# Kernel tuning notes

Hardware: AMD Instinct MI355X
Metric: run time of the kernel (lower is better)

## Reference

```python
import jax, jax.numpy as jnp
import numpy as np

NP_ = 20000   # paper nodes
NA_ = 20000   # author nodes
E_AP = 400000
E_PP = 400000
D_IN, D_H, HEADS, D_HEAD, D_FF, D_OUT = 128, 256, 8, 32, 2048, 64


def setup_inputs() -> dict:
    key = jax.random.key(0)
    ks = iter(jax.random.split(key, 48))
    def nrm(shape, s=0.1):
        return jax.random.normal(next(ks), shape, jnp.float32) * s
    inp = {
        'feat_paper': nrm((NP_, D_IN), 1.0),
        'feat_author': nrm((NA_, D_IN), 1.0),
        'W_in_p': nrm((D_H, D_IN)), 'b_in_p': nrm((D_H,), 0.05),
        'W_in_a': nrm((D_H, D_IN)), 'b_in_a': nrm((D_H,), 0.05),
        'W_gat_ap': nrm((D_H, D_H)), 'al_ap': nrm((HEADS, D_HEAD)), 'ar_ap': nrm((HEADS, D_HEAD)), 'b_gat_ap': nrm((D_H,), 0.05),
        'W_gat_pp': nrm((D_H, D_H)), 'al_pp': nrm((HEADS, D_HEAD)), 'ar_pp': nrm((HEADS, D_HEAD)), 'b_gat_pp': nrm((D_H,), 0.05),
        'Wqkv_s': nrm((3 * D_H, D_H)), 'bqkv_s': nrm((3 * D_H,), 0.05), 'Wo_s': nrm((D_H, D_H)), 'bo_s': nrm((D_H,), 0.05),
        'Wqkv_c': nrm((3 * D_H, D_H)), 'bqkv_c': nrm((3 * D_H,), 0.05), 'Wo_c': nrm((D_H, D_H)), 'bo_c': nrm((D_H,), 0.05),
        'W_ff1': nrm((D_FF, D_H)), 'b_ff1': nrm((D_FF,), 0.05),
        'W_ff2': nrm((D_H, D_FF)), 'b_ff2': nrm((D_H,), 0.05),
        'ln1_g': jnp.ones((D_H,), jnp.float32), 'ln1_b': jnp.zeros((D_H,), jnp.float32),
        'ln2_g': jnp.ones((D_H,), jnp.float32), 'ln2_b': jnp.zeros((D_H,), jnp.float32),
        'ln3_g': jnp.ones((D_H,), jnp.float32), 'ln3_b': jnp.zeros((D_H,), jnp.float32),
        'W_pred': nrm((D_OUT, 3 * D_H)), 'b_pred': nrm((D_OUT,), 0.05),
        'ap_src': jax.random.randint(next(ks), (E_AP,), 0, NA_),
        'ap_dst': jax.random.randint(next(ks), (E_AP,), 0, NP_),
        'pp_src': jax.random.randint(next(ks), (E_PP,), 0, NP_),
        'pp_dst': jax.random.randint(next(ks), (E_PP,), 0, NP_),
    }
    return inp


def _leaky(x):
    return jnp.where(x > 0, x, 0.2 * x)  # DGL GATConv negative_slope=0.2


def _gat(x, src, dst, W, al, ar, b):
    """DGL GATConv on homogeneous graph with self-loops appended (eval mode)."""
    N = x.shape[0]
    h = (x @ W.T).reshape(N, HEADS, D_HEAD)          # fc has no bias in GATConv
    el = (h * al[None]).sum(-1)                      # (N, H)
    er = (h * ar[None]).sum(-1)                      # (N, H)
    sl = jnp.arange(N, dtype=src.dtype)              # self loops (add_self_loop)
    s = jnp.concatenate([src, sl])
    d = jnp.concatenate([dst, sl])
    e = _leaky(el[s] + er[d])                        # (E+N, H)
    m = jax.ops.segment_max(e, d, num_segments=N)    # edge-softmax per dst
    a = jnp.exp(e - m[d])
    z = jax.ops.segment_sum(a, d, num_segments=N)
    out = jax.ops.segment_sum(a[:, :, None] * h[s], d, num_segments=N)
    out = out / z[:, :, None] + b.reshape(1, HEADS, D_HEAD)
    return out.reshape(N, D_H)                       # flatten(start_dim=1)


def _ln(x, g, b):
    mu = x.mean(-1, keepdims=True)
    v = ((x - mu) ** 2).mean(-1, keepdims=True)
    return (x - mu) / jnp.sqrt(v + 1e-5) * g + b


def _mha(xq, xkv, Wqkv, bqkv, Wo, bo):
    Wq, Wk, Wv = jnp.split(Wqkv, 3, axis=0)
    bq, bk, bv = jnp.split(bqkv, 3)
    B, S, _ = xq.shape
    Sk = xkv.shape[1]
    q = (xq @ Wq.T + bq).reshape(B, S, HEADS, D_HEAD)
    k = (xkv @ Wk.T + bk).reshape(B, Sk, HEADS, D_HEAD)
    v = (xkv @ Wv.T + bv).reshape(B, Sk, HEADS, D_HEAD)
    att = jnp.einsum('bqhd,bkhd->bhqk', q, k) * (D_HEAD ** -0.5)
    a = jax.nn.softmax(att, axis=-1)
    o = jnp.einsum('bhqk,bkhd->bqhd', a, v).reshape(B, S, D_H)
    return o @ Wo.T + bo


def reference(feat_paper, feat_author, W_in_p, b_in_p, W_in_a, b_in_a,
              W_gat_ap, al_ap, ar_ap, b_gat_ap, W_gat_pp, al_pp, ar_pp, b_gat_pp,
              Wqkv_s, bqkv_s, Wo_s, bo_s, Wqkv_c, bqkv_c, Wo_c, bo_c,
              W_ff1, b_ff1, W_ff2, b_ff2, ln1_g, ln1_b, ln2_g, ln2_b, ln3_g, ln3_b,
              W_pred, b_pred, ap_src, ap_dst, pp_src, pp_dst):
    # fc_in per node type
    hp = feat_paper @ W_in_p.T + b_in_p              # (NP, D_H)
    ha = feat_author @ W_in_a.T + b_in_a             # (NA, D_H)
    Na = ha.shape[0]
    # etype 'ap': bipartite author->paper, to_homogeneous orders [author; paper]
    x_ap = jnp.concatenate([ha, hp], axis=0)
    out_ap = _gat(x_ap, ap_src, ap_dst + Na, W_gat_ap, al_ap, ar_ap, b_gat_ap)[Na:]
    # etype 'pp': paper->paper (single node set)
    out_pp = _gat(hp, pp_src, pp_dst, W_gat_pp, al_pp, ar_pp, b_gat_pp)
    # h dict order: 'paper', 'paper-author', 'paper-paper'
    tgt = jnp.stack([hp, out_ap, out_pp], axis=1)    # (NP, 3, D_H)
    # TransformerDecoderLayer (post-norm, relu, eval): memory = tgt
    x = _ln(tgt + _mha(tgt, tgt, Wqkv_s, bqkv_s, Wo_s, bo_s), ln1_g, ln1_b)
    x = _ln(x + _mha(x, tgt, Wqkv_c, bqkv_c, Wo_c, bo_c), ln2_g, ln2_b)
    ff = jax.nn.relu(x @ W_ff1.T + b_ff1) @ W_ff2.T + b_ff2
    z = _ln(x + ff, ln3_g, ln3_b)
    return z.reshape(z.shape[0], -1) @ W_pred.T + b_pred
```

## Files before the change

### kernel.cpp

```cpp
#include <hip/hip_runtime.h>
#include <hip/hip_bf16.h>
#include <cstdint>
#include <cstddef>

#define NP_N 20000
#define NA_N 20000
#define E_AP_N 400000
#define E_PP_N 400000

typedef __attribute__((ext_vector_type(8))) short bf16x8;
typedef __attribute__((ext_vector_type(4))) float f32x4;

__device__ __forceinline__ float b2f(ushort u) { return __uint_as_float(((uint32_t)u) << 16); }
__device__ __forceinline__ ushort f2b(float f) {
    uint32_t x = __float_as_uint(f);
    return (ushort)((x + 0x7fffu + ((x >> 16) & 1u)) >> 16);
}

#define LGKM_BARRIER() do { \
    asm volatile("s_waitcnt lgkmcnt(0)" ::: "memory"); \
    __builtin_amdgcn_s_barrier(); \
    __builtin_amdgcn_sched_barrier(0); \
} while (0)

#define NJOBS 14
struct PackJobs {
    const float* src[NJOBS];
    void* dst[NJOBS];
    int M[NJOBS], K[NJOBS];
    int type[NJOBS];
    int nquad[NJOBS];
    int blk0[NJOBS];
};

__global__ void pack_all_kernel(PackJobs J)
{
    int b = blockIdx.x;
    int j = 0;
    while (j + 1 < NJOBS && b >= J.blk0[j + 1]) ++j;
    int u = (b - J.blk0[j]) * 256 + threadIdx.x;
    if (u >= J.nquad[j]) return;
    int ty = J.type[j];
    const float* src = J.src[j];
    if (ty == 3) {
        float4 v = ((const float4*)src)[u];
        ushort4 o;
        o.x = f2b(v.x); o.y = f2b(v.y); o.z = f2b(v.z); o.w = f2b(v.w);
        ((ushort4*)J.dst[j])[u] = o;
    } else if (ty == 4) {
        int4 z = {0, 0, 0, 0};
        ((int4*)J.dst[j])[u] = z;
    } else if (ty == 0) {
        int M = J.M[j], K = J.K[j];
        int KT = K >> 5;
        int q = u & 1023;
        int jt = u >> 10;
        int t = jt % KT, jj = jt / KT;
        int ks = q >> 8, rem = q & 255;
        int r = rem >> 1;
        int e0 = (rem & 1) * 4;
        int row = jj * 128 + r;
        ushort4 o = {0, 0, 0, 0};
        if (row < M) {
            const float* s = src + (size_t)row * K + t * 32 + ks * 8 + e0;
            o.x = f2b(s[0]); o.y = f2b(s[1]); o.z = f2b(s[2]); o.w = f2b(s[3]);
        }
        ((ushort4*)J.dst[j])[u] = o;
    } else if (ty == 1) {
        int q = u & 2047, chunk = u >> 11;
        int s = q >> 6, rem = q & 63;
        int fl = rem >> 1, e0 = (rem & 1) * 4;
        const float* sp = src + (size_t)(chunk * 32 + fl) * 256 + s * 8 + e0;
        ushort4 o;
        o.x = f2b(sp[0]); o.y = f2b(sp[1]); o.z = f2b(sp[2]); o.w = f2b(sp[3]);
        ((ushort4*)J.dst[j])[u] = o;
    } else {
        int q = u & 2047, chunk = u >> 11;
        int s2 = q >> 9, rem = q & 511;
        int c = rem >> 1, e0 = (rem & 1) * 4;
        const float* sp = src + (size_t)c * 2048 + chunk * 32 + s2 * 8 + e0;
        ushort4 o;
        o.x = f2b(sp[0]); o.y = f2b(sp[1]); o.z = f2b(sp[2]); o.w = f2b(sp[3]);
        ((ushort4*)J.dst[j])[u] = o;
    }
}

__device__ __forceinline__ void gemm_body_bf16(
    ushort* Ab, ushort* Bb,
    const ushort* A, const ushort* Bp, const float* bias, ushort* C,
    int N, int M, int K, int lda, int ldc, int row0, int col0)
{
    const int tid = threadIdx.x;
    const int lane = tid & 63;
    const int w = tid >> 6;
    const int wr = w >> 1, wc = w & 1;
    const int KT = K >> 5;
    const ushort* Bbase = Bp + (size_t)(col0 >> 7) * KT * 4096;
    f32x4 acc[4][4] = {};

    size_t aoff[2];
#pragma unroll
    for (int i = 0; i < 2; ++i) {
        int r = row0 + i * 64 + lane;
        if (r > N - 1) r = N - 1;
        aoff[i] = (size_t)r * lda + w * 8;
    }

    auto stage = [&](int buf, int t) {
        const int k0 = t << 5;
#pragma unroll
        for (int i = 0; i < 2; ++i) {
            __builtin_amdgcn_global_load_lds(
                (const __attribute__((address_space(1))) void*)(A + aoff[i] + k0),
                (__attribute__((address_space(3))) void*)(&Ab[buf * 4096 + (w * 2 + i) * 512]), 16, 0, 0);
        }
#pragma unroll
        for (int i = 0; i < 2; ++i) {
            __builtin_amdgcn_global_load_lds(
                (const __attribute__((address_space(1))) void*)(Bbase + (size_t)t * 4096 + (w * 2 + i) * 512 + lane * 8),
                (__attribute__((address_space(3))) void*)(&Bb[buf * 4096 + (w * 2 + i) * 512]), 16, 0, 0);
        }
    };

    stage(0, 0);
    stage(1, 1);

    int cur = 0;
    for (int t = 0; t < KT; ++t) {
        if (t + 1 < KT) { asm volatile("s_waitcnt vmcnt(4)" ::: "memory"); }
        else            { asm volatile("s_waitcnt vmcnt(0)" ::: "memory"); }
        __builtin_amdgcn_s_barrier();
        __builtin_amdgcn_sched_barrier(0);
        if (t + 2 < KT) {
            int nb = cur - 1; if (nb < 0) nb = 2;
            stage(nb, t + 2);
        }

        bf16x8 af[4], bfr[4];
        const int ks = lane >> 4;
        const int rl = lane & 15;
#pragma unroll
        for (int m = 0; m < 4; ++m)
            af[m] = *(const bf16x8*)&Ab[cur * 4096 + ks * 1024 + (wr * 64 + m * 16 + rl) * 8];
#pragma unroll
        for (int n = 0; n < 4; ++n)
            bfr[n] = *(const bf16x8*)&Bb[cur * 4096 + ks * 1024 + (wc * 64 + n * 16 + rl) * 8];
#pragma unroll
        for (int m = 0; m < 4; ++m)
#pragma unroll
            for (int n = 0; n < 4; ++n)
                acc[m][n] = __builtin_amdgcn_mfma_f32_16x16x32_bf16(af[m], bfr[n], acc[m][n], 0, 0, 0);

        cur = (cur == 2) ? 0 : cur + 1;
    }

#pragma unroll
    for (int m = 0; m < 4; ++m) {
#pragma unroll
        for (int n = 0; n < 4; ++n) {
            int gc = col0 + wc * 64 + n * 16 + (lane & 15);
            if (gc >= M) continue;
            float bv = bias ? bias[gc] : 0.f;
#pragma unroll
            for (int r = 0; r < 4; ++r) {
                int grow = row0 + wr * 64 + m * 16 + (lane >> 4) * 4 + r;
                if (grow >= N) continue;
                C[(size_t)grow * ldc + gc] = f2b(acc[m][n][r] + bv);
            }
        }
    }
}

template <int OUT_MODE>
__global__ __launch_bounds__(256) void gemm_mfma(
    const ushort* __restrict__ A, const ushort* __restrict__ Bp,
    const float* __restrict__ bias, void* __restrict__ Cv,
    int N, int M, int K, int lda, int ldc)
{
    __shared__ __align__(16) ushort Ab[3 * 4096];
    __shared__ __align__(16) ushort Bb[3 * 4096];
    if (OUT_MODE == 0) {
        gemm_body_bf16(Ab, Bb, A, Bp, bias, (ushort*)Cv, N, M, K, lda, ldc,
                       blockIdx.x * 128, blockIdx.y * 128);
        return;
    }
    const int tid = threadIdx.x;
    const int lane = tid & 63;
    const int w = tid >> 6;
    const int wr = w >> 1, wc = w & 1;
    const int row0 = blockIdx.x * 128;
    const int col0 = blockIdx.y * 128;
    const int KT = K >> 5;
    const ushort* Bbase = Bp + (size_t)blockIdx.y * KT * 4096;
    f32x4 acc[4][4] = {};

    size_t aoff[2];
#pragma unroll
    for (int i = 0; i < 2; ++i) {
        int r = row0 + i * 64 + lane;
        if (r > N - 1) r = N - 1;
        aoff[i] = (size_t)r * lda + w * 8;
    }

    auto stage = [&](int buf, int t) {
        const int k0 = t << 5;
#pragma unroll
        for (int i = 0; i < 2; ++i) {
            __builtin_amdgcn_global_load_lds(
                (const __attribute__((address_space(1))) void*)(A + aoff[i] + k0),
                (__attribute__((address_space(3))) void*)(&Ab[buf * 4096 + (w * 2 + i) * 512]), 16, 0, 0);
        }
#pragma unroll
        for (int i = 0; i < 2; ++i) {
            __builtin_amdgcn_global_load_lds(
                (const __attribute__((address_space(1))) void*)(Bbase + (size_t)t * 4096 + (w * 2 + i) * 512 + lane * 8),
                (__attribute__((address_space(3))) void*)(&Bb[buf * 4096 + (w * 2 + i) * 512]), 16, 0, 0);
        }
    };

    stage(0, 0);
    stage(1, 1);

    int cur = 0;
    for (int t = 0; t < KT; ++t) {
        if (t + 1 < KT) { asm volatile("s_waitcnt vmcnt(4)" ::: "memory"); }
        else            { asm volatile("s_waitcnt vmcnt(0)" ::: "memory"); }
        __builtin_amdgcn_s_barrier();
        __builtin_amdgcn_sched_barrier(0);
        if (t + 2 < KT) {
            int nb = cur - 1; if (nb < 0) nb = 2;
            stage(nb, t + 2);
        }

        bf16x8 af[4], bfr[4];
        const int ks = lane >> 4;
        const int rl = lane & 15;
#pragma unroll
        for (int m = 0; m < 4; ++m)
            af[m] = *(const bf16x8*)&Ab[cur * 4096 + ks * 1024 + (wr * 64 + m * 16 + rl) * 8];
#pragma unroll
        for (int n = 0; n < 4; ++n)
            bfr[n] = *(const bf16x8*)&Bb[cur * 4096 + ks * 1024 + (wc * 64 + n * 16 + rl) * 8];
#pragma unroll
        for (int m = 0; m < 4; ++m)
#pragma unroll
            for (int n = 0; n < 4; ++n)
                acc[m][n] = __builtin_amdgcn_mfma_f32_16x16x32_bf16(af[m], bfr[n], acc[m][n], 0, 0, 0);

        cur = (cur == 2) ? 0 : cur + 1;
    }

#pragma unroll
    for (int m = 0; m < 4; ++m) {
#pragma unroll
        for (int n = 0; n < 4; ++n) {
            int gc = col0 + wc * 64 + n * 16 + (lane & 15);
            if (gc >= M) continue;
            float bv = bias ? bias[gc] : 0.f;
#pragma unroll
            for (int r = 0; r < 4; ++r) {
                int grow = row0 + wr * 64 + m * 16 + (lane >> 4) * 4 + r;
                if (grow >= N) continue;
                ((float*)Cv)[(size_t)grow * ldc + gc] = acc[m][n][r] + bv;
            }
        }
    }
}

static inline void gemm_bf(const ushort* A, const ushort* Bp, const float* bias, void* C,
                           int N, int M, int K, int lda, int ldc, int mode, hipStream_t s)
{
    dim3 g((N + 127) / 128, (M + 127) / 128);
    if (mode == 0) gemm_mfma<0><<<g, 256, 0, s>>>(A, Bp, bias, C, N, M, K, lda, ldc);
    else           gemm_mfma<1><<<g, 256, 0, s>>>(A, Bp, bias, C, N, M, K, lda, ldc);
}

#define GNJ 3
struct GemmJobs {
    const ushort* A[GNJ];
    const ushort* Bp[GNJ];
    const float* bias[GNJ];
    ushort* C[GNJ];
    int N[GNJ], M[GNJ], K[GNJ], lda[GNJ], ldc[GNJ];
    int blk0[GNJ], nbx[GNJ];
    int njobs;
};

__global__ __launch_bounds__(256) void gemm_batch_kernel(GemmJobs G)
{
    __shared__ __align__(16) ushort Ab[3 * 4096];
    __shared__ __align__(16) ushort Bb[3 * 4096];
    int b = blockIdx.x;
    int j = 0;
    while (j + 1 < G.njobs && b >= G.blk0[j + 1]) ++j;
    int lb = b - G.blk0[j];
    int bx = lb % G.nbx[j];
    int by = lb / G.nbx[j];
    gemm_body_bf16(Ab, Bb, G.A[j], G.Bp[j], G.bias[j], G.C[j],
                   G.N[j], G.M[j], G.K[j], G.lda[j], G.ldc[j], bx * 128, by * 128);
}

__global__ __launch_bounds__(256, 2) void proj_ln_kernel(
    const ushort* o, int ldo,
    const ushort* __restrict__ Bp, const float* __restrict__ bo,
    const ushort* res, int ldr,
    const float* __restrict__ g, const float* __restrict__ be,
    ushort* X, int N)
{
    __shared__ __align__(16) ushort Wb[8192];
    const int tid = threadIdx.x;
    const int lane = tid & 63;
    const int w = tid >> 6;
    const int wr = w >> 1, wc = w & 1;
    const int row0 = blockIdx.x * 64;
    const int rl = lane & 15;
    const int ks = lane >> 4;

    int arow[2];
#pragma unroll
    for (int m = 0; m < 2; ++m) {
        int r = row0 + wr * 32 + m * 16 + rl;
        arow[m] = (r < N) ? r : (N - 1);
    }

    f32x4 oacc[2][8] = {};

    for (int t = 0; t < 8; ++t) {
#pragma unroll
        for (int i = 0; i < 4; ++i) {
            int ii = w * 4 + i;
            const ushort* src = Bp + ((size_t)(ii >> 3) * 8 + t) * 4096 + (ii & 7) * 512 + lane * 8;
            __builtin_amdgcn_global_load_lds(
                (const __attribute__((address_space(1))) void*)src,
                (__attribute__((address_space(3))) void*)(&Wb[ii * 512]), 16, 0, 0);
        }
        bf16x8 af[2];
#pragma unroll
        for (int m = 0; m < 2; ++m)
            af[m] = *(const bf16x8*)(o + (size_t)arow[m] * ldo + t * 32 + ks * 8);
        __syncthreads();

#pragma unroll
        for (int n = 0; n < 8; ++n) {
            bf16x8 bfr = *(const bf16x8*)&Wb[wc * 4096 + ks * 1024 + (n * 16 + rl) * 8];
#pragma unroll
            for (int m = 0; m < 2; ++m)
                oacc[m][n] = __builtin_amdgcn_mfma_f32_16x16x32_bf16(af[m], bfr, oacc[m][n], 0, 0, 0);
        }
        __syncthreads();
    }

    float2* lnb = (float2*)Wb;
    float psum[2][4] = {}, psq[2][4] = {};
#pragma unroll
    for (int n = 0; n < 8; ++n) {
        int c = wc * 128 + n * 16 + rl;
        float bv = bo[c];
#pragma unroll
        for (int m = 0; m < 2; ++m)
#pragma unroll
            for (int r = 0; r < 4; ++r) {
                int grow = row0 + wr * 32 + m * 16 + ks * 4 + r;
                float v = oacc[m][n][r] + bv + b2f(res[(size_t)grow * ldr + c]);
                oacc[m][n][r] = v;
                psum[m][r] += v;
                psq[m][r] = fmaf(v, v, psq[m][r]);
            }
    }
#pragma unroll
    for (int off = 8; off >= 1; off >>= 1)
#pragma unroll
        for (int m = 0; m < 2; ++m)
#pragma unroll
            for (int r = 0; r < 4; ++r) {
                psum[m][r] += __shfl_xor(psum[m][r], off);
                psq[m][r]  += __shfl_xor(psq[m][r], off);
            }
    if (rl == 0) {
#pragma unroll
        for (int m = 0; m < 2; ++m)
#pragma unroll
            for (int r = 0; r < 4; ++r) {
                int lr = wr * 32 + m * 16 + ks * 4 + r;
                lnb[wc * 64 + lr] = make_float2(psum[m][r], psq[m][r]);
            }
    }
    __syncthreads();
    float mean_[2][4], rstd_[2][4];
#pragma unroll
    for (int m = 0; m < 2; ++m)
#pragma unroll
        for (int r = 0; r < 4; ++r) {
            int lr = wr * 32 + m * 16 + ks * 4 + r;
            float2 a0 = lnb[lr], a1 = lnb[64 + lr];
            float mean = (a0.x + a1.x) * (1.f / 256.f);
            float var = (a0.y + a1.y) * (1.f / 256.f) - mean * mean;
            mean_[m][r] = mean;
            rstd_[m][r] = rsqrtf(var + 1e-5f);
        }
#pragma unroll
    for (int n = 0; n < 8; ++n) {
        int c = wc * 128 + n * 16 + rl;
        float gv = g[c], bev = be[c];
#pragma unroll
        for (int m = 0; m < 2; ++m)
#pragma unroll
            for (int r = 0; r < 4; ++r) {
                int grow = row0 + wr * 32 + m * 16 + ks * 4 + r;
                if (grow < N)
                    X[(size_t)grow * 256 + c] =
                        f2b((oacc[m][n][r] - mean_[m][r]) * rstd_[m][r] * gv + bev);
            }
    }
}

__global__ __launch_bounds__(256, 2) void ff_ln_kernel(
    const ushort* __restrict__ W1p, const ushort* __restrict__ W2p,
    const float* __restrict__ b1, const float* __restrict__ b2,
    const float* __restrict__ g3, const float* __restrict__ be3,
    ushort* X, int N)
{
    __shared__ __align__(16) ushort W1buf[8192];
    __shared__ __align__(16) ushort W2buf[8192];
    __shared__ __align__(16) ushort Sbuf[2048];
    const int tid = threadIdx.x;
    const int lane = tid & 63;
    const int w = tid >> 6;
    const int wr = w >> 1, wc = w & 1;
    const int row0 = blockIdx.x * 64;
    const int rl = lane & 15;
    const int ks = lane >> 4;

    bf16x8 xf[2][8];
#pragma unroll
    for (int m = 0; m < 2; ++m) {
        int gr = row0 + wr * 32 + m * 16 + rl;
        if (gr > N - 1) gr = N - 1;
        const ushort* xrow = X + (size_t)gr * 256 + ks * 8;
#pragma unroll
        for (int kc = 0; kc < 8; ++kc)
            xf[m][kc] = *(const bf16x8*)(xrow + kc * 32);
    }

    f32x4 oacc[2][8] = {};

    for (int fc = 0; fc < 64; ++fc) {
#pragma unroll
        for (int i = 0; i < 8; ++i) {
            int ii = w * 8 + i;
            const ushort* src;
            ushort* dst;
            if (ii < 16) {
                src = W1p + (size_t)fc * 8192 + ii * 512 + lane * 8;
                dst = &W1buf[ii * 512];
            } else {
                src = W2p + (size_t)fc * 8192 + (ii - 16) * 512 + lane * 8;
                dst = &W2buf[(ii - 16) * 512];
            }
            __builtin_amdgcn_global_load_lds(
                (const __attribute__((address_space(1))) void*)src,
                (__attribute__((address_space(3))) void*)dst, 16, 0, 0);
        }
        __syncthreads();

        f32x4 sacc[2] = {};
#pragma unroll
        for (int kc = 0; kc < 8; ++kc) {
            bf16x8 w1f = *(const bf16x8*)&W1buf[(kc * 4 + ks) * 256 + (wc * 16 + rl) * 8];
#pragma unroll
            for (int m = 0; m < 2; ++m)
                sacc[m] = __builtin_amdgcn_mfma_f32_16x16x32_bf16(w1f, xf[m][kc], sacc[m], 0, 0, 0);
        }
        {
            const int f0 = fc * 32;
            const int fb = wc * 16 + ks * 4;
            const int sidx = wc * 2 + (ks >> 1);
            const int e0 = (ks & 1) * 4;
            float4 b1v = *(const float4*)&b1[f0 + fb];
#pragma unroll
            for (int m = 0; m < 2; ++m) {
                ushort4 o;
                o.x = f2b(fmaxf(sacc[m][0] + b1v.x, 0.f));
                o.y = f2b(fmaxf(sacc[m][1] + b1v.y, 0.f));
                o.z = f2b(fmaxf(sacc[m][2] + b1v.z, 0.f));
                o.w = f2b(fmaxf(sacc[m][3] + b1v.w, 0.f));
                *(ushort4*)&Sbuf[(sidx * 64 + wr * 32 + m * 16 + rl) * 8 + e0] = o;
            }
        }
        LGKM_BARRIER();

        {
            bf16x8 sf[2];
#pragma unroll
            for (int m = 0; m < 2; ++m)
                sf[m] = *(const bf16x8*)&Sbuf[ks * 512 + (wr * 32 + m * 16 + rl) * 8];
#pragma unroll
            for (int n = 0; n < 8; ++n) {
                bf16x8 w2f = *(const bf16x8*)&W2buf[ks * 2048 + (wc * 128 + n * 16 + rl) * 8];
#pragma unroll
                for (int m = 0; m < 2; ++m)
                    oacc[m][n] = __builtin_amdgcn_mfma_f32_16x16x32_bf16(sf[m], w2f, oacc[m][n], 0, 0, 0);
            }
        }
        __syncthreads();
    }

    float2* lnb = (float2*)W1buf;
    float psum[2][4] = {}, psq[2][4] = {};
#pragma unroll
    for (int n = 0; n < 8; ++n) {
        int c = wc * 128 + n * 16 + rl;
        float bv = b2[c];
#pragma unroll
        for (int m = 0; m < 2; ++m)
#pragma unroll
            for (int r = 0; r < 4; ++r) {
                int grow = row0 + wr * 32 + m * 16 + ks * 4 + r;
                float v = oacc[m][n][r] + bv + b2f(X[(size_t)grow * 256 + c]);
                oacc[m][n][r] = v;
                psum[m][r] += v;
                psq[m][r] = fmaf(v, v, psq[m][r]);
            }
    }
#pragma unroll
    for (int off = 8; off >= 1; off >>= 1)
#pragma unroll
        for (int m = 0; m < 2; ++m)
#pragma unroll
            for (int r = 0; r < 4; ++r) {
                psum[m][r] += __shfl_xor(psum[m][r], off);
                psq[m][r]  += __shfl_xor(psq[m][r], off);
            }
    if (rl == 0) {
#pragma unroll
        for (int m = 0; m < 2; ++m)
#pragma unroll
            for (int r = 0; r < 4; ++r) {
                int lr = wr * 32 + m * 16 + ks * 4 + r;
                lnb[wc * 64 + lr] = make_float2(psum[m][r], psq[m][r]);
            }
    }
    __syncthreads();
    float mean_[2][4], rstd_[2][4];
#pragma unroll
    for (int m = 0; m < 2; ++m)
#pragma unroll
        for (int r = 0; r < 4; ++r) {
            int lr = wr * 32 + m * 16 + ks * 4 + r;
            float2 a0 = lnb[lr], a1 = lnb[64 + lr];
            float mean = (a0.x + a1.x) * (1.f / 256.f);
            float var = (a0.y + a1.y) * (1.f / 256.f) - mean * mean;
            mean_[m][r] = mean;
            rstd_[m][r] = rsqrtf(var + 1e-5f);
        }
#pragma unroll
    for (int n = 0; n < 8; ++n) {
        int c = wc * 128 + n * 16 + rl;
        float gv = g3[c], bev = be3[c];
#pragma unroll
        for (int m = 0; m < 2; ++m)
#pragma unroll
            for (int r = 0; r < 4; ++r) {
                int grow = row0 + wr * 32 + m * 16 + ks * 4 + r;
                if (grow < N)
                    X[(size_t)grow * 256 + c] =
                        f2b((oacc[m][n][r] - mean_[m][r]) * rstd_[m][r] * gv + bev);
            }
    }
}

__global__ void attn_lr_all_kernel(
    const ushort* __restrict__ h0, const float* __restrict__ al0, const float* __restrict__ ar0,
    float* __restrict__ el0, float* __restrict__ er0,
    const ushort* __restrict__ h1, const float* __restrict__ al1, const float* __restrict__ ar1,
    float* __restrict__ el1, float* __restrict__ er1)
{
    int idx = blockIdx.x * blockDim.x + threadIdx.x;
    if (idx >= 480000) return;
    const ushort* h; const float *a1, *a2; float *el, *er; int i;
    if (idx < 320000) { h = h0; a1 = al0; a2 = ar0; el = el0; er = er0; i = idx; }
    else { h = h1; a1 = al1; a2 = ar1; el = el1; er = er1; i = idx - 320000; }
    int hd = i & 7;
    const ushort* hp = h + (size_t)(i >> 3) * 256 + hd * 32;
    const float* p1 = a1 + hd * 32;
    const float* p2 = a2 + hd * 32;
    float s1 = 0.f, s2 = 0.f;
#pragma unroll
    for (int j = 0; j < 8; ++j) {
        ushort4 t = ((const ushort4*)hp)[j];
        float v0 = b2f(t.x), v1 = b2f(t.y), v2 = b2f(t.z), v3 = b2f(t.w);
        s1 = fmaf(v0, p1[j * 4 + 0], s1); s2 = fmaf(v0, p2[j * 4 + 0], s2);
        s1 = fmaf(v1, p1[j * 4 + 1], s1); s2 = fmaf(v1, p2[j * 4 + 1], s2);
        s1 = fmaf(v2, p1[j * 4 + 2], s1); s2 = fmaf(v2, p2[j * 4 + 2], s2);
        s1 = fmaf(v3, p1[j * 4 + 3], s1); s2 = fmaf(v3, p2[j * 4 + 3], s2);
    }
    el[i] = s1;
    er[i] = s2;
}

__global__ void count2_kernel(const int* __restrict__ d0, int* __restrict__ c0,
                              const int* __restrict__ d1, int* __restrict__ c1, int E)
{
    int e = blockIdx.x * blockDim.x + threadIdx.x;
    if (e < E) atomicAdd(&c0[d0[e]], 1);
    else if (e < 2 * E) atomicAdd(&c1[d1[e - E]], 1);
}

__global__ void scan_chunk_kernel(const int* __restrict__ deg0, int* __restrict__ offs0,
                                  const int* __restrict__ deg1, int* __restrict__ offs1,
                                  int* __restrict__ parts, int N)
{
    int es = blockIdx.x / 20, ch = blockIdx.x % 20;
    const int* deg = es ? deg1 : deg0;
    int* offs = es ? offs1 : offs0;
    __shared__ int sbuf[1024];
    int tid = threadIdx.x;
    int i = ch * 1024 + tid;
    int v = (i < N) ? deg[i] : 0;
    sbuf[tid] = v;
    __syncthreads();
    for (int off = 1; off < 1024; off <<= 1) {
        int t = (tid >= off) ? sbuf[tid - off] : 0;
        __syncthreads();
        sbuf[tid] += t;
        __syncthreads();
    }
    if (i < N) offs[i] = sbuf[tid] - v;
    if (tid == 1023) parts[es * 21 + ch] = sbuf[1023];
}

__global__ void scan_final_kernel(int* __restrict__ deg0, int* __restrict__ offs0,
                                  int* __restrict__ deg1, int* __restrict__ offs1,
                                  const int* __restrict__ parts, int N)
{
    int es = blockIdx.x / 20, ch = blockIdx.x % 20;
    int* deg = es ? deg1 : deg0;
    int* offs = es ? offs1 : offs0;
    __shared__ int base_s, tot_s;
    int tid = threadIdx.x;
    if (tid == 0) {
        const int* p = parts + es * 21;
        int acc = 0, base = 0;
        for (int i = 0; i < 20; ++i) { if (i == ch) base = acc; acc += p[i]; }
        base_s = base;
        tot_s = acc;
    }
    __syncthreads();
    int i = ch * 1024 + tid;
    if (i < N) { offs[i] += base_s; deg[i] = 0; }
    if (ch == 19 && tid == 1023) offs[N] = tot_s;
}

__global__ void scatter2_kernel(const int* __restrict__ s0, const int* __restrict__ d0,
                                const int* __restrict__ o0, int* __restrict__ c0, int* __restrict__ l0,
                                const int* __restrict__ s1, const int* __restrict__ d1,
                                const int* __restrict__ o1, int* __restrict__ c1, int* __restrict__ l1,
                                int E)
{
    int e = blockIdx.x * blockDim.x + threadIdx.x;
    if (e < E) {
        int d = d0[e];
        int pos = atomicAdd(&c0[d], 1);
        l0[o0[d] + pos] = s0[e];
    } else if (e < 2 * E) {
        int e1 = e - E;
        int d = d1[e1];
        int pos = atomicAdd(&c1[d], 1);
        l1[o1[d] + pos] = s1[e1];
    }
}

__global__ __launch_bounds__(64) void gat_agg_all_kernel(
    const ushort* __restrict__ ha, const float* __restrict__ ela, const float* __restrict__ era,
    const int* __restrict__ offsa, const int* __restrict__ lista, const float* __restrict__ biasa,
    const ushort* __restrict__ hp, const float* __restrict__ elp, const float* __restrict__ erp,
    const int* __restrict__ offsp, const int* __restrict__ listp, const float* __restrict__ biasp,
    ushort* __restrict__ out)
{
    int bid = blockIdx.x;
    const ushort* h; const float *el, *er, *bias; const int *offs, *elist;
    int p, dn, coloff;
    if (bid < NP_N) {
        h = ha; el = ela; er = era; offs = offsa; elist = lista; bias = biasa;
        p = bid; dn = NA_N + p; coloff = 256;
    } else {
        h = hp; el = elp; er = erp; offs = offsp; elist = listp; bias = biasp;
        p = bid - NP_N; dn = p; coloff = 512;
    }
    int l = threadIdx.x;
    int head = l >> 3;
    float erv = er[(size_t)dn * 8 + head];
    float acc[4] = {0.f, 0.f, 0.f, 0.f};
    float z = 0.f;
    int beg = offs[p], end = offs[p + 1];
    for (int e = beg - 1; e < end; ++e) {
        int s = (e < beg) ? dn : elist[e];
        float x = el[(size_t)s * 8 + head] + erv;
        x = x > 0.f ? x : 0.2f * x;
        float wgt = expf(x);
        z += wgt;
        ushort4 hv = *(const ushort4*)&h[(size_t)s * 256 + l * 4];
        acc[0] = fmaf(wgt, b2f(hv.x), acc[0]);
        acc[1] = fmaf(wgt, b2f(hv.y), acc[1]);
        acc[2] = fmaf(wgt, b2f(hv.z), acc[2]);
        acc[3] = fmaf(wgt, b2f(hv.w), acc[3]);
    }
    float inv = 1.f / z;
    ushort4 o;
    o.x = f2b(acc[0] * inv + bias[l * 4 + 0]);
    o.y = f2b(acc[1] * inv + bias[l * 4 + 1]);
    o.z = f2b(acc[2] * inv + bias[l * 4 + 2]);
    o.w = f2b(acc[3] * inv + bias[l * 4 + 3]);
    *(ushort4*)&out[(size_t)p * 768 + coloff + l * 4] = o;
}

__global__ void mha3_kernel(const ushort* qb, int ldq, int qoff,
                            const ushort* kvb, int ldkv, int koff, int voff,
                            ushort* ob, int ldo, int NPn)
{
    int idx = blockIdx.x * blockDim.x + threadIdx.x;
    if (idx >= NPn * 24) return;
    int h = idx & 7;
    int i = (idx >> 3) % 3;
    int p = idx / 24;
    float qr[32];
    {
        const ushort* q = qb + (size_t)(p * 3 + i) * ldq + qoff + h * 32;
#pragma unroll
        for (int j = 0; j < 8; ++j) {
            ushort4 t = ((const ushort4*)q)[j];
            qr[j * 4 + 0] = b2f(t.x); qr[j * 4 + 1] = b2f(t.y);
            qr[j * 4 + 2] = b2f(t.z); qr[j * 4 + 3] = b2f(t.w);
        }
    }
    float s[3];
#pragma unroll
    for (int j = 0; j < 3; ++j) {
        const ushort* k = kvb + (size_t)(p * 3 + j) * ldkv + koff + h * 32;
        float a = 0.f;
#pragma unroll
        for (int t4 = 0; t4 < 8; ++t4) {
            ushort4 t = ((const ushort4*)k)[t4];
            a = fmaf(qr[t4 * 4 + 0], b2f(t.x), a);
            a = fmaf(qr[t4 * 4 + 1], b2f(t.y), a);
            a = fmaf(qr[t4 * 4 + 2], b2f(t.z), a);
            a = fmaf(qr[t4 * 4 + 3], b2f(t.w), a);
        }
        s[j] = a * 0.17677669529663687f;
    }
    float m = fmaxf(s[0], fmaxf(s[1], s[2]));
    float e0 = expf(s[0] - m), e1 = expf(s[1] - m), e2 = expf(s[2] - m);
    float inv = 1.f / (e0 + e1 + e2);
    float aw[3] = {e0 * inv, e1 * inv, e2 * inv};
    float o[32] = {};
#pragma unroll
    for (int j = 0; j < 3; ++j) {
        const ushort* v = kvb + (size_t)(p * 3 + j) * ldkv + voff + h * 32;
#pragma unroll
        for (int t4 = 0; t4 < 8; ++t4) {
            ushort4 t = ((const ushort4*)v)[t4];
            o[t4 * 4 + 0] = fmaf(aw[j], b2f(t.x), o[t4 * 4 + 0]);
            o[t4 * 4 + 1] = fmaf(aw[j], b2f(t.y), o[t4 * 4 + 1]);
            o[t4 * 4 + 2] = fmaf(aw[j], b2f(t.z), o[t4 * 4 + 2]);
            o[t4 * 4 + 3] = fmaf(aw[j], b2f(t.w), o[t4 * 4 + 3]);
        }
    }
    ushort* op = ob + (size_t)(p * 3 + i) * ldo + h * 32;
#pragma unroll
    for (int t4 = 0; t4 < 8; ++t4) {
        ushort4 t;
        t.x = f2b(o[t4 * 4 + 0]); t.y = f2b(o[t4 * 4 + 1]);
        t.z = f2b(o[t4 * 4 + 2]); t.w = f2b(o[t4 * 4 + 3]);
        ((ushort4*)op)[t4] = t;
    }
}

extern "C" void kernel_launch(void* const* d_in, const int* in_sizes, int n_in,
                              void* d_out, int out_size, void* d_ws, size_t ws_size,
                              hipStream_t stream)
{
    const float* feat_paper  = (const float*)d_in[0];
    const float* feat_author = (const float*)d_in[1];
    const float* W_in_p  = (const float*)d_in[2];
    const float* b_in_p  = (const float*)d_in[3];
    const float* W_in_a  = (const float*)d_in[4];
    const float* b_in_a  = (const float*)d_in[5];
    const float* W_gat_ap = (const float*)d_in[6];
    const float* al_ap    = (const float*)d_in[7];
    const float* ar_ap    = (const float*)d_in[8];
    const float* b_gat_ap = (const float*)d_in[9];
    const float* W_gat_pp = (const float*)d_in[10];
    const float* al_pp    = (const float*)d_in[11];
    const float* ar_pp    = (const float*)d_in[12];
    const float* b_gat_pp = (const float*)d_in[13];
    const float* Wqkv_s = (const float*)d_in[14];
    const float* bqkv_s = (const float*)d_in[15];
    const float* Wo_s   = (const float*)d_in[16];
    const float* bo_s   = (const float*)d_in[17];
    const float* Wqkv_c = (const float*)d_in[18];
    const float* bqkv_c = (const float*)d_in[19];
    const float* Wo_c   = (const float*)d_in[20];
    const float* bo_c   = (const float*)d_in[21];
    const float* W_ff1  = (const float*)d_in[22];
    const float* b_ff1  = (const float*)d_in[23];
    const float* W_ff2  = (const float*)d_in[24];
    const float* b_ff2  = (const float*)d_in[25];
    const float* ln1_g  = (const float*)d_in[26];
    const float* ln1_b  = (const float*)d_in[27];
    const float* ln2_g  = (const float*)d_in[28];
    const float* ln2_b  = (const float*)d_in[29];
    const float* ln3_g  = (const float*)d_in[30];
    const float* ln3_b  = (const float*)d_in[31];
    const float* W_pred = (const float*)d_in[32];
    const float* b_pred = (const float*)d_in[33];
    const int* ap_src = (const int*)d_in[34];
    const int* ap_dst = (const int*)d_in[35];
    const int* pp_src = (const int*)d_in[36];
    const int* pp_dst = (const int*)d_in[37];

    const int NP = NP_N, NA = NA_N;

    uint8_t* wsb = (uint8_t*)d_ws;
    ushort* tgt_bf = (ushort*)wsb;
    ushort* X_bf   = (ushort*)(wsb + 30720000);
    ushort* WB     = (ushort*)(wsb + 61440000);
    ushort* p_in_p   = WB + 0;
    ushort* p_in_a   = WB + 32768;
    ushort* p_gat_ap = WB + 65536;
    ushort* p_gat_pp = WB + 131072;
    ushort* p_qkv_s  = WB + 196608;
    ushort* p_o_s    = WB + 393216;
    ushort* p_qkv_c  = WB + 458752;
    ushort* p_o_c    = WB + 655360;
    ushort* p_pred   = WB + 720896;
    ushort* p_ff1    = WB + 819200;
    ushort* p_ff2    = WB + 1343488;
    uint8_t* BIG = wsb + 65280000;

    ushort* feat_p_bf = (ushort*)BIG;
    ushort* feat_a_bf = (ushort*)(BIG + 5120000);
    ushort* x_ap_bf   = (ushort*)(BIG + 10240000);
    ushort* h_ap_bf   = (ushort*)(BIG + 30720000);
    ushort* h_pp_bf   = (ushort*)(BIG + 51200000);
    float* el_ap = (float*)(BIG + 61440000);
    float* er_ap = (float*)(BIG + 62720000);
    float* el_pp = (float*)(BIG + 64000000);
    float* er_pp = (float*)(BIG + 64640000);
    int* ireg    = (int*)(BIG + 65280000);
    int* ap_offs = ireg;
    int* pp_offs = ireg + 20004;
    int* ap_cur  = ireg + 40008;
    int* pp_cur  = ireg + 60008;
    int* ap_list = ireg + 80008;
    int* pp_list = ireg + 480008;
    int* parts   = ireg + 880008;

    {
        PackJobs J;
        const float* srcs[NJOBS] = { feat_paper, feat_author, W_in_p, W_in_a, W_gat_ap,
                                     W_gat_pp, Wqkv_s, Wo_s, Wqkv_c, Wo_c, W_pred,
                                     W_ff1, W_ff2, nullptr };
        void* dsts[NJOBS] = { feat_p_bf, feat_a_bf, p_in_p, p_in_a, p_gat_ap,
                              p_gat_pp, p_qkv_s, p_o_s, p_qkv_c, p_o_c, p_pred,
                              p_ff1, p_ff2, ap_cur };
        int Ms[NJOBS]  = {0,0, 256,256,256,256, 768,256,768,256, 64, 0,0, 0};
        int Ks[NJOBS]  = {0,0, 128,128,256,256, 256,256,256,256, 768, 0,0, 0};
        int tys[NJOBS] = {3,3, 0,0,0,0, 0,0,0,0, 0, 1,2, 4};
        int nq[NJOBS]  = {640000,640000, 8192,8192,16384,16384, 49152,16384,49152,16384,
                          24576, 131072,131072, 10000};
        int acc = 0;
        for (int j = 0; j < NJOBS; ++j) {
            J.src[j] = srcs[j]; J.dst[j] = dsts[j];
            J.M[j] = Ms[j]; J.K[j] = Ks[j]; J.type[j] = tys[j]; J.nquad[j] = nq[j];
            J.blk0[j] = acc;
            acc += (nq[j] + 255) / 256;
        }
        pack_all_kernel<<<acc, 256, 0, stream>>>(J);
    }

    {
        GemmJobs G;
        G.njobs = 2;
        G.A[0] = feat_a_bf; G.Bp[0] = p_in_a; G.bias[0] = b_in_a; G.C[0] = x_ap_bf;
        G.N[0] = NA; G.M[0] = 256; G.K[0] = 128; G.lda[0] = 128; G.ldc[0] = 256;
        G.A[1] = feat_p_bf; G.Bp[1] = p_in_p; G.bias[1] = b_in_p; G.C[1] = tgt_bf;
        G.N[1] = NP; G.M[1] = 256; G.K[1] = 128; G.lda[1] = 128; G.ldc[1] = 768;
        int acc = 0;
        for (int j = 0; j < 2; ++j) {
            G.nbx[j] = (G.N[j] + 127) / 128;
            G.blk0[j] = acc;
            acc += G.nbx[j] * ((G.M[j] + 127) / 128);
        }
        gemm_batch_kernel<<<acc, 256, 0, stream>>>(G);
    }

    {
        GemmJobs G;
        G.njobs = 3;
        G.A[0] = x_ap_bf; G.Bp[0] = p_gat_ap; G.bias[0] = nullptr; G.C[0] = h_ap_bf;
        G.N[0] = NA; G.M[0] = 256; G.K[0] = 256; G.lda[0] = 256; G.ldc[0] = 256;
        G.A[1] = tgt_bf; G.Bp[1] = p_gat_ap; G.bias[1] = nullptr; G.C[1] = h_ap_bf + (size_t)NA * 256;
        G.N[1] = NP; G.M[1] = 256; G.K[1] = 256; G.lda[1] = 768; G.ldc[1] = 256;
        G.A[2] = tgt_bf; G.Bp[2] = p_gat_pp; G.bias[2] = nullptr; G.C[2] = h_pp_bf;
        G.N[2] = NP; G.M[2] = 256; G.K[2] = 256; G.lda[2] = 768; G.ldc[2] = 256;
        int acc = 0;
        for (int j = 0; j < 3; ++j) {
            G.nbx[j] = (G.N[j] + 127) / 128;
            G.blk0[j] = acc;
            acc += G.nbx[j] * ((G.M[j] + 127) / 128);
        }
        gemm_batch_kernel<<<acc, 256, 0, stream>>>(G);
    }

    attn_lr_all_kernel<<<1875, 256, 0, stream>>>(h_ap_bf, al_ap, ar_ap, el_ap, er_ap,
                                                 h_pp_bf, al_pp, ar_pp, el_pp, er_pp);

    count2_kernel<<<3125, 256, 0, stream>>>(ap_dst, ap_cur, pp_dst, pp_cur, E_AP_N);
    scan_chunk_kernel<<<40, 1024, 0, stream>>>(ap_cur, ap_offs, pp_cur, pp_offs, parts, NP);
    scan_final_kernel<<<40, 1024, 0, stream>>>(ap_cur, ap_offs, pp_cur, pp_offs, parts, NP);
    scatter2_kernel<<<3125, 256, 0, stream>>>(ap_src, ap_dst, ap_offs, ap_cur, ap_list,
                                              pp_src, pp_dst, pp_offs, pp_cur, pp_list, E_AP_N);

    gat_agg_all_kernel<<<2 * NP, 64, 0, stream>>>(
        h_ap_bf, el_ap, er_ap, ap_offs, ap_list, b_gat_ap,
        h_pp_bf, el_pp, er_pp, pp_offs, pp_list, b_gat_pp, tgt_bf);

    {
        ushort* qkv = (ushort*)BIG;
        gemm_bf(tgt_bf, p_qkv_s, bqkv_s, qkv, 60000, 768, 256, 256, 768, 0, stream);
        mha3_kernel<<<(NP * 24 + 255) / 256, 256, 0, stream>>>(qkv, 768, 0, qkv, 768, 256, 512, qkv, 768, NP);
        proj_ln_kernel<<<(60000 + 63) / 64, 256, 0, stream>>>(
            qkv, 768, p_o_s, bo_s, tgt_bf, 256, ln1_g, ln1_b, X_bf, 60000);
    }

    {
        ushort* qb  = (ushort*)BIG;
        ushort* kvb = (ushort*)(BIG + 30720000);
        const ushort* p_kv_c = p_qkv_c + (size_t)2 * 8 * 4096;
        GemmJobs G;
        G.njobs = 2;
        G.A[0] = X_bf; G.Bp[0] = p_qkv_c; G.bias[0] = bqkv_c; G.C[0] = qb;
        G.N[0] = 60000; G.M[0] = 256; G.K[0] = 256; G.lda[0] = 256; G.ldc[0] = 256;
        G.A[1] = tgt_bf; G.Bp[1] = p_kv_c; G.bias[1] = bqkv_c + 256; G.C[1] = kvb;
        G.N[1] = 60000; G.M[1] = 512; G.K[1] = 256; G.lda[1] = 256; G.ldc[1] = 512;
        int acc = 0;
        for (int j = 0; j < 2; ++j) {
            G.nbx[j] = (G.N[j] + 127) / 128;
            G.blk0[j] = acc;
            acc += G.nbx[j] * ((G.M[j] + 127) / 128);
        }
        gemm_batch_kernel<<<acc, 256, 0, stream>>>(G);
        mha3_kernel<<<(NP * 24 + 255) / 256, 256, 0, stream>>>(qb, 256, 0, kvb, 512, 0, 256, qb, 256, NP);
        proj_ln_kernel<<<(60000 + 63) / 64, 256, 0, stream>>>(
            qb, 256, p_o_c, bo_c, X_bf, 256, ln2_g, ln2_b, X_bf, 60000);
    }

    ff_ln_kernel<<<(60000 + 63) / 64, 256, 0, stream>>>(p_ff1, p_ff2, b_ff1, b_ff2,
                                                        ln3_g, ln3_b, X_bf, 60000);

    gemm_bf(X_bf, p_pred, b_pred, (float*)d_out, NP, 64, 768, 768, 64, 1, stream);
}
```

Measured before the change: 747.2 us.

## Fuse 3-token attention into output-projection+LayerNorm kernel via LDS staging

Removes the standalone mha3 kernel and computes each row's 3-key attention inside the projection+LayerNorm kernel. The per-head attention output goes to a padded shared-memory tile, which feeds the MFMA output projection directly. This drops one global write and re-read of the attention output and one launch per attention block. In exchange it adds about 33 KB of LDS per block, which may cut occupancy below the launch-bounds target, and it raises register pressure from the 32-float attention arrays.

```diff
diff --git a/kernel.cpp b/kernel.cpp
--- a/kernel.cpp
+++ b/kernel.cpp
@@ -300,14 +300,16 @@
                    G.N[j], G.M[j], G.K[j], G.lda[j], G.ldc[j], bx * 128, by * 128);
 }
 
-__global__ __launch_bounds__(256, 2) void proj_ln_kernel(
-    const ushort* o, int ldo,
+__global__ __launch_bounds__(256, 2) void attn_proj_ln_kernel(
+    const ushort* qb, int ldq, int qoff,
+    const ushort* kvb, int ldkv, int koff, int voff,
     const ushort* __restrict__ Bp, const float* __restrict__ bo,
     const ushort* res, int ldr,
     const float* __restrict__ g, const float* __restrict__ be,
     ushort* X, int N)
 {
     __shared__ __align__(16) ushort Wb[8192];
+    __shared__ __align__(16) ushort obuf[64 * 264];
     const int tid = threadIdx.x;
     const int lane = tid & 63;
     const int w = tid >> 6;
@@ -323,6 +325,68 @@
         arow[m] = (r < N) ? r : (N - 1);
     }
 
+#pragma unroll
+    for (int m = 0; m < 2; ++m) {
+        int r = arow[m];
+        int pb = r - (r % 3);
+        int lr = wr * 32 + m * 16 + rl;
+#pragma unroll
+        for (int hh = 0; hh < 2; ++hh) {
+            int h = ks * 2 + hh;
+            float qr[32];
+            {
+                const ushort* q = qb + (size_t)r * ldq + qoff + h * 32;
+#pragma unroll
+                for (int j = 0; j < 8; ++j) {
+                    ushort4 t = ((const ushort4*)q)[j];
+                    qr[j * 4 + 0] = b2f(t.x); qr[j * 4 + 1] = b2f(t.y);
+                    qr[j * 4 + 2] = b2f(t.z); qr[j * 4 + 3] = b2f(t.w);
+                }
+            }
+            float s[3];
+#pragma unroll
+            for (int j = 0; j < 3; ++j) {
+                const ushort* k = kvb + (size_t)(pb + j) * ldkv + koff + h * 32;
+                float a = 0.f;
+#pragma unroll
+                for (int t4 = 0; t4 < 8; ++t4) {
+                    ushort4 t = ((const ushort4*)k)[t4];
+                    a = fmaf(qr[t4 * 4 + 0], b2f(t.x), a);
+                    a = fmaf(qr[t4 * 4 + 1], b2f(t.y), a);
+                    a = fmaf(qr[t4 * 4 + 2], b2f(t.z), a);
+                    a = fmaf(qr[t4 * 4 + 3], b2f(t.w), a);
+                }
+                s[j] = a * 0.17677669529663687f;
+            }
+            float mx = fmaxf(s[0], fmaxf(s[1], s[2]));
+            float e0 = expf(s[0] - mx), e1 = expf(s[1] - mx), e2 = expf(s[2] - mx);
+            float inv = 1.f / (e0 + e1 + e2);
+            float aw[3] = {e0 * inv, e1 * inv, e2 * inv};
+            float o[32] = {};
+#pragma unroll
+            for (int j = 0; j < 3; ++j) {
+                const ushort* v = kvb + (size_t)(pb + j) * ldkv + voff + h * 32;
+#pragma unroll
+                for (int t4 = 0; t4 < 8; ++t4) {
+                    ushort4 t = ((const ushort4*)v)[t4];
+                    o[t4 * 4 + 0] = fmaf(aw[j], b2f(t.x), o[t4 * 4 + 0]);
+                    o[t4 * 4 + 1] = fmaf(aw[j], b2f(t.y), o[t4 * 4 + 1]);
+                    o[t4 * 4 + 2] = fmaf(aw[j], b2f(t.z), o[t4 * 4 + 2]);
+                    o[t4 * 4 + 3] = fmaf(aw[j], b2f(t.w), o[t4 * 4 + 3]);
+                }
+            }
+            ushort* op = &obuf[lr * 264 + h * 32];
+#pragma unroll
+            for (int t4 = 0; t4 < 8; ++t4) {
+                ushort4 t;
+                t.x = f2b(o[t4 * 4 + 0]); t.y = f2b(o[t4 * 4 + 1]);
+                t.z = f2b(o[t4 * 4 + 2]); t.w = f2b(o[t4 * 4 + 3]);
+                ((ushort4*)op)[t4] = t;
+            }
+        }
+    }
+    __syncthreads();
+
     f32x4 oacc[2][8] = {};
 
     for (int t = 0; t < 8; ++t) {
@@ -337,7 +401,7 @@
         bf16x8 af[2];
 #pragma unroll
         for (int m = 0; m < 2; ++m)
-            af[m] = *(const bf16x8*)(o + (size_t)arow[m] * ldo + t * 32 + ks * 8);
+            af[m] = *(const bf16x8*)&obuf[(wr * 32 + m * 16 + rl) * 264 + t * 32 + ks * 8];
         __syncthreads();
 
 #pragma unroll
@@ -712,67 +776,6 @@
     o.z = f2b(acc[2] * inv + bias[l * 4 + 2]);
     o.w = f2b(acc[3] * inv + bias[l * 4 + 3]);
     *(ushort4*)&out[(size_t)p * 768 + coloff + l * 4] = o;
-}
-
-__global__ void mha3_kernel(const ushort* qb, int ldq, int qoff,
-                            const ushort* kvb, int ldkv, int koff, int voff,
-                            ushort* ob, int ldo, int NPn)
-{
-    int idx = blockIdx.x * blockDim.x + threadIdx.x;
-    if (idx >= NPn * 24) return;
-    int h = idx & 7;
-    int i = (idx >> 3) % 3;
-    int p = idx / 24;
-    float qr[32];
-    {
-        const ushort* q = qb + (size_t)(p * 3 + i) * ldq + qoff + h * 32;
-#pragma unroll
-        for (int j = 0; j < 8; ++j) {
-            ushort4 t = ((const ushort4*)q)[j];
-            qr[j * 4 + 0] = b2f(t.x); qr[j * 4 + 1] = b2f(t.y);
-            qr[j * 4 + 2] = b2f(t.z); qr[j * 4 + 3] = b2f(t.w);
-        }
-    }
-    float s[3];
-#pragma unroll
-    for (int j = 0; j < 3; ++j) {
-        const ushort* k = kvb + (size_t)(p * 3 + j) * ldkv + koff + h * 32;
-        float a = 0.f;
-#pragma unroll
-        for (int t4 = 0; t4 < 8; ++t4) {
-            ushort4 t = ((const ushort4*)k)[t4];
-            a = fmaf(qr[t4 * 4 + 0], b2f(t.x), a);
-            a = fmaf(qr[t4 * 4 + 1], b2f(t.y), a);
-            a = fmaf(qr[t4 * 4 + 2], b2f(t.z), a);
-            a = fmaf(qr[t4 * 4 + 3], b2f(t.w), a);
-        }
-        s[j] = a * 0.17677669529663687f;
-    }
-    float m = fmaxf(s[0], fmaxf(s[1], s[2]));
-    float e0 = expf(s[0] - m), e1 = expf(s[1] - m), e2 = expf(s[2] - m);
-    float inv = 1.f / (e0 + e1 + e2);
-    float aw[3] = {e0 * inv, e1 * inv, e2 * inv};
-    float o[32] = {};
-#pragma unroll
-    for (int j = 0; j < 3; ++j) {
-        const ushort* v = kvb + (size_t)(p * 3 + j) * ldkv + voff + h * 32;
-#pragma unroll
-        for (int t4 = 0; t4 < 8; ++t4) {
-            ushort4 t = ((const ushort4*)v)[t4];
-            o[t4 * 4 + 0] = fmaf(aw[j], b2f(t.x), o[t4 * 4 + 0]);
-            o[t4 * 4 + 1] = fmaf(aw[j], b2f(t.y), o[t4 * 4 + 1]);
-            o[t4 * 4 + 2] = fmaf(aw[j], b2f(t.z), o[t4 * 4 + 2]);
-            o[t4 * 4 + 3] = fmaf(aw[j], b2f(t.w), o[t4 * 4 + 3]);
-        }
-    }
-    ushort* op = ob + (size_t)(p * 3 + i) * ldo + h * 32;
-#pragma unroll
-    for (int t4 = 0; t4 < 8; ++t4) {
-        ushort4 t;
-        t.x = f2b(o[t4 * 4 + 0]); t.y = f2b(o[t4 * 4 + 1]);
-        t.z = f2b(o[t4 * 4 + 2]); t.w = f2b(o[t4 * 4 + 3]);
-        ((ushort4*)op)[t4] = t;
-    }
 }
 
 extern "C" void kernel_launch(void* const* d_in, const int* in_sizes, int n_in,
@@ -928,9 +931,9 @@
     {
         ushort* qkv = (ushort*)BIG;
         gemm_bf(tgt_bf, p_qkv_s, bqkv_s, qkv, 60000, 768, 256, 256, 768, 0, stream);
-        mha3_kernel<<<(NP * 24 + 255) / 256, 256, 0, stream>>>(qkv, 768, 0, qkv, 768, 256, 512, qkv, 768, NP);
-        proj_ln_kernel<<<(60000 + 63) / 64, 256, 0, stream>>>(
-            qkv, 768, p_o_s, bo_s, tgt_bf, 256, ln1_g, ln1_b, X_bf, 60000);
+        attn_proj_ln_kernel<<<(60000 + 63) / 64, 256, 0, stream>>>(
+            qkv, 768, 0, qkv, 768, 256, 512,
+            p_o_s, bo_s, tgt_bf, 256, ln1_g, ln1_b, X_bf, 60000);
     }
 
     {
@@ -950,9 +953,9 @@
             acc += G.nbx[j] * ((G.M[j] + 127) / 128);
         }
         gemm_batch_kernel<<<acc, 256, 0, stream>>>(G);
-        mha3_kernel<<<(NP * 24 + 255) / 256, 256, 0, stream>>>(qb, 256, 0, kvb, 512, 0, 256, qb, 256, NP);
-        proj_ln_kernel<<<(60000 + 63) / 64, 256, 0, stream>>>(
-            qb, 256, p_o_c, bo_c, X_bf, 256, ln2_g, ln2_b, X_bf, 60000);
+        attn_proj_ln_kernel<<<(60000 + 63) / 64, 256, 0, stream>>>(
+            qb, 256, 0, kvb, 512, 0, 256,
+            p_o_c, bo_c, X_bf, 256, ln2_g, ln2_b, X_bf, 60000);
     }
 
     ff_ln_kernel<<<(60000 + 63) / 64, 256, 0, stream>>>(p_ff1, p_ff2, b_ff1, b_ff2,
```

After: 755.5 us. About the same (+1.1%).
